# Kernel optimization log

Hardware: AMD Instinct MI355X
Metric: run time of the kernel (lower is better)

The kernel has to match this reference:

```python
import jax, jax.numpy as jnp
import numpy as np


def setup_inputs() -> dict:
    key = jax.random.key(0)
    ks = jax.random.split(key, 8)
    B, S, H, I = 2, 1025, 3200, 12800
    T = B * S
    # int8 tensors represented as int32, symmetric range [-128, 126]
    hidden_states = jax.random.randint(ks[0], (B, S, H), 0, 255, dtype=jnp.int32) - 127
    scale_in = (jax.random.uniform(ks[1], (T,)) * 0.02 + 1e-4).astype(jnp.float16)
    w1 = jax.random.randint(ks[2], (I, H), 0, 255, dtype=jnp.int32) - 127
    w1_scale = (jax.random.uniform(ks[3], (I,)) * 0.01 + 1e-4).astype(jnp.float32)
    b1 = (jax.random.normal(ks[4], (I,)) * 0.02).astype(jnp.float16)
    w2 = jax.random.randint(ks[5], (H, I), 0, 255, dtype=jnp.int32) - 127
    w2_scale = (jax.random.uniform(ks[6], (H,)) * 0.01 + 1e-4).astype(jnp.float32)
    b2 = (jax.random.normal(ks[7], (H,)) * 0.02).astype(jnp.float16)
    return {"hidden_states": hidden_states, "scale_in": scale_in,
            "w1": w1, "w1_scale": w1_scale, "b1": b1,
            "w2": w2, "w2_scale": w2_scale, "b2": b2}


def _w8a8_linear(x_int, scale_x, w_int, w_scale, bias):
    # int8 GEMM with int32 accumulation, dequant with per-token * per-channel scales
    acc = jnp.matmul(x_int, w_int.T)  # [T, out] int32
    out = acc.astype(jnp.float32) * scale_x[:, None].astype(jnp.float32) * w_scale[None, :]
    return (out + bias.astype(jnp.float32)).astype(jnp.float16)


def _gelu_and_quant(x_f16):
    # fused GELU + per-token dynamic symmetric int8 quantization
    g = jax.nn.gelu(x_f16.astype(jnp.float32), approximate=False)  # [T, I]
    amax = jnp.max(jnp.abs(g), axis=-1)                              # [T]
    scale_act = (amax / 127.0).astype(jnp.float16)
    s = jnp.maximum(scale_act.astype(jnp.float32), 1e-8)
    q = jnp.clip(jnp.round(g / s[:, None]), -128, 127).astype(jnp.int32)
    return q, scale_act


def reference(hidden_states, scale_in, w1, w1_scale, b1, w2, w2_scale, b2):
    B, S, H = hidden_states.shape
    x = hidden_states.reshape(-1, H)               # [T, H] int
    fc1_out = _w8a8_linear(x, scale_in, w1, w1_scale, b1)      # [T, I] fp16
    act_out, scale_act = _gelu_and_quant(fc1_out)              # int8-as-int32, [T] fp16
    fc2_out = _w8a8_linear(act_out, scale_act, w2, w2_scale, b2)  # [T, H] fp16
    return fc2_out
```

## Files before the change

### kernel.cpp

```cpp
#include <hip/hip_runtime.h>
#include <hip/hip_fp16.h>

typedef int v4i __attribute__((ext_vector_type(4)));

#define AS1C(p) ((const __attribute__((address_space(1))) void*)(p))
#define AS3(p)  ((__attribute__((address_space(3))) void*)(p))

__device__ __forceinline__ void stage_tile(const signed char* __restrict__ g, long long ld,
                                           long long rmax, long long r0, int k0,
                                           char* lds, int tid) {
  const int wave = tid >> 6, lane = tid & 63;
#pragma unroll
  for (int p = 0; p < 2; ++p) {
    const int chunk = wave * 2 + p;
    const int row = chunk * 16 + (lane >> 2);
    const int slot = lane & 3;
    const int gslot = slot ^ ((row >> 1) & 3);
    long long rg = r0 + row;
    if (rg > rmax) rg = rmax;
    const signed char* src = g + rg * ld + (long long)k0 + gslot * 16;
    char* dst = lds + chunk * 1024;
    __builtin_amdgcn_global_load_lds(AS1C(src), AS3(dst), 16, 0, 0);
  }
}

template <int EPI>
__launch_bounds__(256, 4)
__global__ void gemm_i8(const signed char* __restrict__ A, const signed char* __restrict__ Bw,
                        int M, int N, int K,
                        const float* __restrict__ scale_tok, const float* __restrict__ wsc,
                        const float* __restrict__ bias,
                        __half* __restrict__ gout, unsigned int* __restrict__ amax,
                        float* __restrict__ fout) {
  __shared__ __align__(16) char lds[2][2][128 * 64];
  const int tid = threadIdx.x;
  const int lane = tid & 63, wave = tid >> 6;
  const int wrow = (wave >> 1) * 64, wcol = (wave & 1) * 64;

  const int gy = gridDim.y;
  int lid;
  {
    const int o = blockIdx.y * gridDim.x + blockIdx.x;
    const int nwg = gridDim.x * gy;
    const int q = nwg >> 3, r = nwg & 7;
    const int x = o & 7, p = o >> 3;
    lid = (x < r ? x * (q + 1) : r * (q + 1) + (x - r) * q) + p;
  }
  const long long t0 = (long long)(lid % gy) * 128;
  const long long n0 = (long long)(lid / gy) * 128;

  v4i acc[4][4] = {};

  stage_tile(A, K, (long long)M - 1, t0, 0, lds[0][0], tid);
  stage_tile(Bw, K, (long long)N - 1, n0, 0, lds[0][1], tid);
  __syncthreads();

  const int nk = K >> 6;
  int cur = 0;
  const int srow = lane & 15, sseg = lane >> 4;
  for (int kt = 0; kt < nk; ++kt) {
    if (kt + 1 < nk) {
      stage_tile(A, K, (long long)M - 1, t0, (kt + 1) << 6, lds[cur ^ 1][0], tid);
      stage_tile(Bw, K, (long long)N - 1, n0, (kt + 1) << 6, lds[cur ^ 1][1], tid);
    }
    v4i af[4], bf[4];
#pragma unroll
    for (int mi = 0; mi < 4; ++mi) {
      const int r = wrow + mi * 16 + srow;
      const int sl = sseg ^ ((r >> 1) & 3);
      af[mi] = *(const v4i*)&lds[cur][0][r * 64 + sl * 16];
    }
#pragma unroll
    for (int ni = 0; ni < 4; ++ni) {
      const int r = wcol + ni * 16 + srow;
      const int sl = sseg ^ ((r >> 1) & 3);
      bf[ni] = *(const v4i*)&lds[cur][1][r * 64 + sl * 16];
    }
#pragma unroll
    for (int mi = 0; mi < 4; ++mi)
#pragma unroll
      for (int ni = 0; ni < 4; ++ni)
        acc[mi][ni] = __builtin_amdgcn_mfma_i32_16x16x64_i8(af[mi], bf[ni], acc[mi][ni], 0, 0, 0);
    __syncthreads();
    cur ^= 1;
  }

  if (EPI == 0) {
#pragma unroll
    for (int mi = 0; mi < 4; ++mi) {
#pragma unroll
      for (int j = 0; j < 4; ++j) {
        const long long t = t0 + wrow + mi * 16 + (lane >> 4) * 4 + j;
        const bool valid = (t < M);
        const float st = valid ? scale_tok[t] : 0.f;
        float rowmax = 0.f;
#pragma unroll
        for (int ni = 0; ni < 4; ++ni) {
          const long long c = n0 + wcol + ni * 16 + (lane & 15);
          float v = (float)acc[mi][ni][j] * st * wsc[c] + bias[c];
          v = __half2float(__float2half(v));
          const float gl = 0.5f * v * (1.f + erff(v * 0.70710678118654752f));
          rowmax = fmaxf(rowmax, fabsf(gl));
          if (valid) gout[t * (long long)N + c] = __float2half(gl);
        }
#pragma unroll
        for (int m = 1; m < 16; m <<= 1) rowmax = fmaxf(rowmax, __shfl_xor(rowmax, m));
        if (valid && (lane & 15) == 0) atomicMax(&amax[t], __float_as_uint(rowmax));
      }
    }
  } else {
#pragma unroll
    for (int mi = 0; mi < 4; ++mi) {
#pragma unroll
      for (int j = 0; j < 4; ++j) {
        const long long t = t0 + wrow + mi * 16 + (lane >> 4) * 4 + j;
        if (t < M) {
          const float am = __uint_as_float(amax[t]);
          const float st = __half2float(__float2half(am * (1.f / 127.f)));
#pragma unroll
          for (int ni = 0; ni < 4; ++ni) {
            const long long c = n0 + wcol + ni * 16 + (lane & 15);
            const float v = (float)acc[mi][ni][j] * st * wsc[c] + bias[c];
            fout[t * (long long)N + c] = __half2float(__float2half(v));
          }
        }
      }
    }
  }
}

__global__ void pack_all(const int* __restrict__ a, const int* __restrict__ b,
                         const int* __restrict__ c,
                         signed char* __restrict__ pa, signed char* __restrict__ pb,
                         signed char* __restrict__ pc,
                         unsigned int* __restrict__ amax,
                         long long na, long long nb, long long nc, int T) {
  const long long gid = blockIdx.x * (long long)blockDim.x + threadIdx.x;
  if (gid < T) amax[gid] = 0u;
  const long long n4a = na >> 2, n4b = nb >> 2, n4c = nc >> 2;
  const long long tot = n4a + n4b + n4c;
  const long long stride = (long long)gridDim.x * blockDim.x;
  for (long long u = gid; u < tot; u += stride) {
    const int* src; signed char* dst; long long loc;
    if (u < n4a)            { src = a; dst = pa; loc = u; }
    else if (u < n4a + n4b) { src = b; dst = pb; loc = u - n4a; }
    else                    { src = c; dst = pc; loc = u - n4a - n4b; }
    const int4 v = *(const int4*)(src + (loc << 2));
    const unsigned out = (unsigned)(v.x & 0xff) | ((unsigned)(v.y & 0xff) << 8) |
                         ((unsigned)(v.z & 0xff) << 16) | ((unsigned)(v.w & 0xff) << 24);
    *(unsigned*)(dst + (loc << 2)) = out;
  }
}

__global__ void gelu_quant(const __half* __restrict__ g, const unsigned int* __restrict__ amax,
                           signed char* __restrict__ q, long long total, int I) {
  const long long nchunk = total >> 3;
  const long long stride = (long long)gridDim.x * blockDim.x;
  for (long long c = blockIdx.x * (long long)blockDim.x + threadIdx.x; c < nchunk; c += stride) {
    const long long base = c << 3;
    const int t = (int)(base / I);
    const float am = __uint_as_float(amax[t]);
    const float s = fmaxf(__half2float(__float2half(am * (1.f / 127.f))), 1e-8f);
    const float inv = 1.f / s;
    const int4 raw = *(const int4*)(g + base);
    const __half2* h2 = (const __half2*)&raw;
    union { signed char b[8]; int2 v; } u;
#pragma unroll
    for (int k = 0; k < 4; ++k) {
      const float2 f = __half22float2(h2[k]);
      const float q0 = fminf(fmaxf(rintf(f.x * inv), -128.f), 127.f);
      const float q1 = fminf(fmaxf(rintf(f.y * inv), -128.f), 127.f);
      u.b[k * 2]     = (signed char)(int)q0;
      u.b[k * 2 + 1] = (signed char)(int)q1;
    }
    *(int2*)(q + base) = u.v;
  }
}

extern "C" void kernel_launch(void* const* d_in, const int* in_sizes, int n_in,
                              void* d_out, int out_size, void* d_ws, size_t ws_size,
                              hipStream_t stream) {
  const int* hs = (const int*)d_in[0];
  const float* scale_in = (const float*)d_in[1];
  const int* w1 = (const int*)d_in[2];
  const float* w1s = (const float*)d_in[3];
  const float* b1 = (const float*)d_in[4];
  const int* w2 = (const int*)d_in[5];
  const float* w2s = (const float*)d_in[6];
  const float* b2 = (const float*)d_in[7];

  const int T = in_sizes[1];
  const int I = in_sizes[3];
  const int H = in_sizes[6];

  char* ws = (char*)d_ws;
  unsigned int* amax = (unsigned int*)ws;
  signed char* px  = (signed char*)(ws + 16384);
  signed char* pw1 = px + (size_t)T * H;
  signed char* pw2 = pw1 + (size_t)I * H;
  __half* gbuf = (__half*)(pw2 + (size_t)H * I);
  signed char* qbuf = (signed char*)(gbuf + (size_t)T * I);

  const long long nx = (long long)T * H, nw1 = (long long)I * H, nw2 = (long long)H * I;

  pack_all<<<2048, 256, 0, stream>>>(hs, w1, w2, px, pw1, pw2, amax, nx, nw1, nw2, T);

  dim3 g1(I / 128, (T + 127) / 128);
  gemm_i8<0><<<g1, 256, 0, stream>>>(px, pw1, T, I, H, scale_in, w1s, b1, gbuf, amax, nullptr);

  gelu_quant<<<2048, 256, 0, stream>>>(gbuf, amax, qbuf, (long long)T * I, I);

  dim3 g2(H / 128, (T + 127) / 128);
  gemm_i8<1><<<g2, 256, 0, stream>>>(qbuf, pw2, T, H, I, nullptr, w2s, b2, nullptr, amax, (float*)d_out);
}
```

Baseline: 380.0 us.

## Reshape GEMM tiles to 64x256 with waves splitting columns and precomputed load pointers

Changes each GEMM workgroup tile from 128x128 to 64 tokens by 256 output channels. All four waves now share the same A rows and each owns a 64-column slice of B. Global-to-LDS staging uses precomputed, incrementally advanced pointers instead of recomputing addresses each k-step, and per-column scale and bias are hoisted out of the epilogue. The tile is aimed at this skinny-M shape: it lowers tile padding waste for T=2050 and changes the A/B traffic ratio. In exchange, B must be re-read from global memory more often (more row tiles), N-bound checks are added for H not divisible by 256, and LDS use per block rises.

Result: slower. 423.9 us (+11.5%).

```diff
diff --git a/kernel.cpp b/kernel.cpp
--- a/kernel.cpp
+++ b/kernel.cpp
@@ -6,36 +6,18 @@
 #define AS1C(p) ((const __attribute__((address_space(1))) void*)(p))
 #define AS3(p)  ((__attribute__((address_space(3))) void*)(p))
 
-__device__ __forceinline__ void stage_tile(const signed char* __restrict__ g, long long ld,
-                                           long long rmax, long long r0, int k0,
-                                           char* lds, int tid) {
-  const int wave = tid >> 6, lane = tid & 63;
-#pragma unroll
-  for (int p = 0; p < 2; ++p) {
-    const int chunk = wave * 2 + p;
-    const int row = chunk * 16 + (lane >> 2);
-    const int slot = lane & 3;
-    const int gslot = slot ^ ((row >> 1) & 3);
-    long long rg = r0 + row;
-    if (rg > rmax) rg = rmax;
-    const signed char* src = g + rg * ld + (long long)k0 + gslot * 16;
-    char* dst = lds + chunk * 1024;
-    __builtin_amdgcn_global_load_lds(AS1C(src), AS3(dst), 16, 0, 0);
-  }
-}
-
 template <int EPI>
 __launch_bounds__(256, 4)
-__global__ void gemm_i8(const signed char* __restrict__ A, const signed char* __restrict__ Bw,
-                        int M, int N, int K,
-                        const float* __restrict__ scale_tok, const float* __restrict__ wsc,
-                        const float* __restrict__ bias,
-                        __half* __restrict__ gout, unsigned int* __restrict__ amax,
-                        float* __restrict__ fout) {
-  __shared__ __align__(16) char lds[2][2][128 * 64];
+__global__ void gemm_w(const signed char* __restrict__ A, const signed char* __restrict__ Bw,
+                       int M, int N, int K,
+                       const float* __restrict__ scale_tok, const float* __restrict__ wsc,
+                       const float* __restrict__ bias,
+                       __half* __restrict__ gout, unsigned int* __restrict__ amax,
+                       float* __restrict__ fout) {
+  __shared__ __align__(16) char smem[2][20480];
   const int tid = threadIdx.x;
   const int lane = tid & 63, wave = tid >> 6;
-  const int wrow = (wave >> 1) * 64, wcol = (wave & 1) * 64;
+  const int lh = lane & 15, sseg = lane >> 4;
 
   const int gy = gridDim.y;
   int lid;
@@ -46,36 +28,56 @@
     const int x = o & 7, p = o >> 3;
     lid = (x < r ? x * (q + 1) : r * (q + 1) + (x - r) * q) + p;
   }
-  const long long t0 = (long long)(lid % gy) * 128;
-  const long long n0 = (long long)(lid / gy) * 128;
+  const long long t0 = (long long)(lid % gy) * 64;
+  const long long n0 = (long long)(lid / gy) * 256;
+  const int nk = K >> 6;
+  const long long Mm1 = M - 1, Nm1 = N - 1;
+
+  const int lr4 = lane >> 2, slot = lane & 3;
+  const signed char* spA;
+  {
+    const int rloc = wave * 16 + lr4;
+    const int gslot = (slot ^ ((rloc >> 1) & 3)) << 4;
+    long long gr = t0 + rloc; if (gr > Mm1) gr = Mm1;
+    spA = A + gr * (long long)K + gslot;
+  }
+  const signed char* spB[4];
+#pragma unroll
+  for (int i = 0; i < 4; ++i) {
+    const int cb = wave * 4 + i;
+    const int rloc = cb * 16 + lr4;
+    const int gslot = (slot ^ ((rloc >> 1) & 3)) << 4;
+    long long gr = n0 + rloc; if (gr > Nm1) gr = Nm1;
+    spB[i] = Bw + gr * (long long)K + gslot;
+  }
+  const int dstA = wave * 1024;
+
+#define STAGE(bi) do { \
+    __builtin_amdgcn_global_load_lds(AS1C(spA), AS3(&smem[bi][dstA]), 16, 0, 0); spA += 64; \
+    _Pragma("unroll") \
+    for (int i = 0; i < 4; ++i) { \
+      __builtin_amdgcn_global_load_lds(AS1C(spB[i]), AS3(&smem[bi][4096 + (wave * 4 + i) * 1024]), 16, 0, 0); \
+      spB[i] += 64; \
+    } \
+  } while (0)
+
+  const int xs = ((sseg ^ ((lh >> 1) & 3)) << 4);
+  const int offA = lh * 64 + xs;
+  const int offB = 4096 + wave * 4096 + lh * 64 + xs;
 
   v4i acc[4][4] = {};
 
-  stage_tile(A, K, (long long)M - 1, t0, 0, lds[0][0], tid);
-  stage_tile(Bw, K, (long long)N - 1, n0, 0, lds[0][1], tid);
+  STAGE(0);
   __syncthreads();
 
-  const int nk = K >> 6;
   int cur = 0;
-  const int srow = lane & 15, sseg = lane >> 4;
   for (int kt = 0; kt < nk; ++kt) {
-    if (kt + 1 < nk) {
-      stage_tile(A, K, (long long)M - 1, t0, (kt + 1) << 6, lds[cur ^ 1][0], tid);
-      stage_tile(Bw, K, (long long)N - 1, n0, (kt + 1) << 6, lds[cur ^ 1][1], tid);
-    }
+    if (kt + 1 < nk) STAGE(cur ^ 1);
     v4i af[4], bf[4];
 #pragma unroll
-    for (int mi = 0; mi < 4; ++mi) {
-      const int r = wrow + mi * 16 + srow;
-      const int sl = sseg ^ ((r >> 1) & 3);
-      af[mi] = *(const v4i*)&lds[cur][0][r * 64 + sl * 16];
-    }
-#pragma unroll
-    for (int ni = 0; ni < 4; ++ni) {
-      const int r = wcol + ni * 16 + srow;
-      const int sl = sseg ^ ((r >> 1) & 3);
-      bf[ni] = *(const v4i*)&lds[cur][1][r * 64 + sl * 16];
-    }
+    for (int mi = 0; mi < 4; ++mi) af[mi] = *(const v4i*)&smem[cur][offA + mi * 1024];
+#pragma unroll
+    for (int ni = 0; ni < 4; ++ni) bf[ni] = *(const v4i*)&smem[cur][offB + ni * 1024];
 #pragma unroll
     for (int mi = 0; mi < 4; ++mi)
 #pragma unroll
@@ -84,28 +86,36 @@
     __syncthreads();
     cur ^= 1;
   }
-
+#undef STAGE
+
+  long long cidx[4]; float w4[4], bi4[4]; bool cok[4];
+#pragma unroll
+  for (int ni = 0; ni < 4; ++ni) {
+    cidx[ni] = n0 + wave * 64 + ni * 16 + lh;
+    cok[ni] = cidx[ni] < N;
+    w4[ni] = cok[ni] ? wsc[cidx[ni]] : 0.f;
+    bi4[ni] = cok[ni] ? bias[cidx[ni]] : 0.f;
+  }
   if (EPI == 0) {
 #pragma unroll
     for (int mi = 0; mi < 4; ++mi) {
 #pragma unroll
       for (int j = 0; j < 4; ++j) {
-        const long long t = t0 + wrow + mi * 16 + (lane >> 4) * 4 + j;
+        const long long t = t0 + mi * 16 + (lane >> 4) * 4 + j;
         const bool valid = (t < M);
         const float st = valid ? scale_tok[t] : 0.f;
         float rowmax = 0.f;
 #pragma unroll
         for (int ni = 0; ni < 4; ++ni) {
-          const long long c = n0 + wcol + ni * 16 + (lane & 15);
-          float v = (float)acc[mi][ni][j] * st * wsc[c] + bias[c];
+          float v = (float)acc[mi][ni][j] * st * w4[ni] + bi4[ni];
           v = __half2float(__float2half(v));
           const float gl = 0.5f * v * (1.f + erff(v * 0.70710678118654752f));
           rowmax = fmaxf(rowmax, fabsf(gl));
-          if (valid) gout[t * (long long)N + c] = __float2half(gl);
+          if (valid && cok[ni]) gout[t * (long long)N + cidx[ni]] = __float2half(gl);
         }
 #pragma unroll
         for (int m = 1; m < 16; m <<= 1) rowmax = fmaxf(rowmax, __shfl_xor(rowmax, m));
-        if (valid && (lane & 15) == 0) atomicMax(&amax[t], __float_as_uint(rowmax));
+        if (valid && lh == 0) atomicMax(&amax[t], __float_as_uint(rowmax));
       }
     }
   } else {
@@ -113,15 +123,14 @@
     for (int mi = 0; mi < 4; ++mi) {
 #pragma unroll
       for (int j = 0; j < 4; ++j) {
-        const long long t = t0 + wrow + mi * 16 + (lane >> 4) * 4 + j;
+        const long long t = t0 + mi * 16 + (lane >> 4) * 4 + j;
         if (t < M) {
           const float am = __uint_as_float(amax[t]);
           const float st = __half2float(__float2half(am * (1.f / 127.f)));
 #pragma unroll
           for (int ni = 0; ni < 4; ++ni) {
-            const long long c = n0 + wcol + ni * 16 + (lane & 15);
-            const float v = (float)acc[mi][ni][j] * st * wsc[c] + bias[c];
-            fout[t * (long long)N + c] = __half2float(__float2half(v));
+            const float v = (float)acc[mi][ni][j] * st * w4[ni] + bi4[ni];
+            if (cok[ni]) fout[t * (long long)N + cidx[ni]] = __half2float(__float2half(v));
           }
         }
       }
@@ -205,11 +214,11 @@
 
   pack_all<<<2048, 256, 0, stream>>>(hs, w1, w2, px, pw1, pw2, amax, nx, nw1, nw2, T);
 
-  dim3 g1(I / 128, (T + 127) / 128);
-  gemm_i8<0><<<g1, 256, 0, stream>>>(px, pw1, T, I, H, scale_in, w1s, b1, gbuf, amax, nullptr);
+  dim3 g1(I / 256, (T + 63) / 64);
+  gemm_w<0><<<g1, 256, 0, stream>>>(px, pw1, T, I, H, scale_in, w1s, b1, gbuf, amax, nullptr);
 
   gelu_quant<<<2048, 256, 0, stream>>>(gbuf, amax, qbuf, (long long)T * I, I);
 
-  dim3 g2(H / 128, (T + 127) / 128);
-  gemm_i8<1><<<g2, 256, 0, stream>>>(qbuf, pw2, T, H, I, nullptr, w2s, b2, nullptr, amax, (float*)d_out);
-}
+  dim3 g2((H + 255) / 256, (T + 63) / 64);
+  gemm_w<1><<<g2, 256, 0, stream>>>(qbuf, pw2, T, H, I, nullptr, w2s, b2, nullptr, amax, (float*)d_out);
+}
```

## Use 256x256 tiles with 1024-thread blocks for the FC1 GEMM

Applied to the files above, without the earlier changes.

Replaces the FC1 int8 GEMM with a new kernel that computes 256x256 output tiles using 16 waves, each wave still holding a 64x64 accumulator block. Larger tiles halve the global traffic per MAC and make each LDS stage reuse more data. Staging pointers are precomputed and advanced by a stride. Per-column scale and bias are hoisted out of the epilogue loop. The risks are fewer workgroups (about 9x50) for the 256 CUs, a tail in the last M tile where T=2050 is padded to 2304, and higher LDS use per block (64 KB). FC2 keeps the old kernel, now specialised without the template.

After: 374.7 us. About the same (-1.4%).

```diff
diff --git a/kernel.cpp b/kernel.cpp
--- a/kernel.cpp
+++ b/kernel.cpp
@@ -5,6 +5,116 @@
 
 #define AS1C(p) ((const __attribute__((address_space(1))) void*)(p))
 #define AS3(p)  ((__attribute__((address_space(3))) void*)(p))
+
+__launch_bounds__(1024, 4)
+__global__ void gemm256(const signed char* __restrict__ A, const signed char* __restrict__ Bw,
+                        int M, int N, int K,
+                        const float* __restrict__ scale_tok, const float* __restrict__ wsc,
+                        const float* __restrict__ bias,
+                        __half* __restrict__ gout, unsigned int* __restrict__ amax) {
+  __shared__ __align__(16) char smem[2][32768];
+  const int tid = threadIdx.x;
+  const int lane = tid & 63, wave = tid >> 6;
+  const int wavem = wave >> 2, waven = wave & 3;
+  const int lh = lane & 15, sseg = lane >> 4;
+
+  const int gy = gridDim.y;
+  int lid;
+  {
+    const int o = blockIdx.y * gridDim.x + blockIdx.x;
+    const int nwg = gridDim.x * gy;
+    const int q = nwg >> 3, r = nwg & 7;
+    const int x = o & 7, p = o >> 3;
+    lid = (x < r ? x * (q + 1) : r * (q + 1) + (x - r) * q) + p;
+  }
+  const long long t0 = (long long)(lid % gy) * 256;
+  const long long n0 = (long long)(lid / gy) * 256;
+  const int nk = K >> 6;
+  const long long Mm1 = M - 1, Nm1 = N - 1;
+
+  const int lr4 = lane >> 2, slot = lane & 3;
+  const int rloc = wave * 16 + lr4;
+  const int gslot = (slot ^ ((rloc >> 1) & 3)) << 4;
+  const signed char* sp0;
+  const signed char* sp1;
+  {
+    long long gr = t0 + rloc; if (gr > Mm1) gr = Mm1;
+    sp0 = A + gr * (long long)K + gslot;
+    long long gn = n0 + rloc; if (gn > Nm1) gn = Nm1;
+    sp1 = Bw + gn * (long long)K + gslot;
+  }
+  const int d0 = wave * 1024, d1 = 16384 + wave * 1024;
+
+#define STAGE(bi) do { \
+    __builtin_amdgcn_global_load_lds(AS1C(sp0), AS3(&smem[bi][d0]), 16, 0, 0); sp0 += 64; \
+    __builtin_amdgcn_global_load_lds(AS1C(sp1), AS3(&smem[bi][d1]), 16, 0, 0); sp1 += 64; \
+  } while (0)
+
+  const int xs = ((sseg ^ ((lh >> 1) & 3)) << 4);
+  const int offA = wavem * 4096 + lh * 64 + xs;
+  const int offB = 16384 + waven * 4096 + lh * 64 + xs;
+
+  v4i acc[4][4] = {};
+
+  STAGE(0);
+  __syncthreads();
+
+  int cur = 0;
+  for (int kt = 0; kt < nk; ++kt) {
+    if (kt + 1 < nk) STAGE(cur ^ 1);
+    const char* base = smem[cur];
+    v4i af[4], bf[2];
+#pragma unroll
+    for (int mi = 0; mi < 4; ++mi) af[mi] = *(const v4i*)(base + offA + mi * 1024);
+    bf[0] = *(const v4i*)(base + offB);
+    bf[1] = *(const v4i*)(base + offB + 1024);
+#pragma unroll
+    for (int mi = 0; mi < 4; ++mi) {
+      acc[mi][0] = __builtin_amdgcn_mfma_i32_16x16x64_i8(af[mi], bf[0], acc[mi][0], 0, 0, 0);
+      acc[mi][1] = __builtin_amdgcn_mfma_i32_16x16x64_i8(af[mi], bf[1], acc[mi][1], 0, 0, 0);
+    }
+    bf[0] = *(const v4i*)(base + offB + 2048);
+    bf[1] = *(const v4i*)(base + offB + 3072);
+#pragma unroll
+    for (int mi = 0; mi < 4; ++mi) {
+      acc[mi][2] = __builtin_amdgcn_mfma_i32_16x16x64_i8(af[mi], bf[0], acc[mi][2], 0, 0, 0);
+      acc[mi][3] = __builtin_amdgcn_mfma_i32_16x16x64_i8(af[mi], bf[1], acc[mi][3], 0, 0, 0);
+    }
+    __syncthreads();
+    cur ^= 1;
+  }
+#undef STAGE
+
+  long long cidx[4]; float w4[4], bi4[4]; bool cok[4];
+#pragma unroll
+  for (int ni = 0; ni < 4; ++ni) {
+    cidx[ni] = n0 + waven * 64 + ni * 16 + lh;
+    cok[ni] = cidx[ni] < N;
+    w4[ni] = cok[ni] ? wsc[cidx[ni]] : 0.f;
+    bi4[ni] = cok[ni] ? bias[cidx[ni]] : 0.f;
+  }
+#pragma unroll
+  for (int mi = 0; mi < 4; ++mi) {
+#pragma unroll
+    for (int j = 0; j < 4; ++j) {
+      const long long t = t0 + wavem * 64 + mi * 16 + (lane >> 4) * 4 + j;
+      const bool valid = t < M;
+      const float st = valid ? scale_tok[t] : 0.f;
+      float rowmax = 0.f;
+#pragma unroll
+      for (int ni = 0; ni < 4; ++ni) {
+        float v = (float)acc[mi][ni][j] * st * w4[ni] + bi4[ni];
+        v = __half2float(__float2half(v));
+        const float gl = 0.5f * v * (1.f + erff(v * 0.70710678118654752f));
+        rowmax = fmaxf(rowmax, fabsf(gl));
+        if (valid && cok[ni]) gout[t * (long long)N + cidx[ni]] = __float2half(gl);
+      }
+#pragma unroll
+      for (int m = 1; m < 16; m <<= 1) rowmax = fmaxf(rowmax, __shfl_xor(rowmax, m));
+      if (valid && lh == 0) atomicMax(&amax[t], __float_as_uint(rowmax));
+    }
+  }
+}
 
 __device__ __forceinline__ void stage_tile(const signed char* __restrict__ g, long long ld,
                                            long long rmax, long long r0, int k0,
@@ -24,14 +134,11 @@
   }
 }
 
-template <int EPI>
 __launch_bounds__(256, 4)
-__global__ void gemm_i8(const signed char* __restrict__ A, const signed char* __restrict__ Bw,
-                        int M, int N, int K,
-                        const float* __restrict__ scale_tok, const float* __restrict__ wsc,
-                        const float* __restrict__ bias,
-                        __half* __restrict__ gout, unsigned int* __restrict__ amax,
-                        float* __restrict__ fout) {
+__global__ void gemm_fc2(const signed char* __restrict__ A, const signed char* __restrict__ Bw,
+                         int M, int N, int K,
+                         const float* __restrict__ wsc, const float* __restrict__ bias,
+                         unsigned int* __restrict__ amax, float* __restrict__ fout) {
   __shared__ __align__(16) char lds[2][2][128 * 64];
   const int tid = threadIdx.x;
   const int lane = tid & 63, wave = tid >> 6;
@@ -85,44 +192,19 @@
     cur ^= 1;
   }
 
-  if (EPI == 0) {
-#pragma unroll
-    for (int mi = 0; mi < 4; ++mi) {
-#pragma unroll
-      for (int j = 0; j < 4; ++j) {
-        const long long t = t0 + wrow + mi * 16 + (lane >> 4) * 4 + j;
-        const bool valid = (t < M);
-        const float st = valid ? scale_tok[t] : 0.f;
-        float rowmax = 0.f;
+#pragma unroll
+  for (int mi = 0; mi < 4; ++mi) {
+#pragma unroll
+    for (int j = 0; j < 4; ++j) {
+      const long long t = t0 + wrow + mi * 16 + (lane >> 4) * 4 + j;
+      if (t < M) {
+        const float am = __uint_as_float(amax[t]);
+        const float st = __half2float(__float2half(am * (1.f / 127.f)));
 #pragma unroll
         for (int ni = 0; ni < 4; ++ni) {
           const long long c = n0 + wcol + ni * 16 + (lane & 15);
-          float v = (float)acc[mi][ni][j] * st * wsc[c] + bias[c];
-          v = __half2float(__float2half(v));
-          const float gl = 0.5f * v * (1.f + erff(v * 0.70710678118654752f));
-          rowmax = fmaxf(rowmax, fabsf(gl));
-          if (valid) gout[t * (long long)N + c] = __float2half(gl);
-        }
-#pragma unroll
-        for (int m = 1; m < 16; m <<= 1) rowmax = fmaxf(rowmax, __shfl_xor(rowmax, m));
-        if (valid && (lane & 15) == 0) atomicMax(&amax[t], __float_as_uint(rowmax));
-      }
-    }
-  } else {
-#pragma unroll
-    for (int mi = 0; mi < 4; ++mi) {
-#pragma unroll
-      for (int j = 0; j < 4; ++j) {
-        const long long t = t0 + wrow + mi * 16 + (lane >> 4) * 4 + j;
-        if (t < M) {
-          const float am = __uint_as_float(amax[t]);
-          const float st = __half2float(__float2half(am * (1.f / 127.f)));
-#pragma unroll
-          for (int ni = 0; ni < 4; ++ni) {
-            const long long c = n0 + wcol + ni * 16 + (lane & 15);
-            const float v = (float)acc[mi][ni][j] * st * wsc[c] + bias[c];
-            fout[t * (long long)N + c] = __half2float(__float2half(v));
-          }
+          const float v = (float)acc[mi][ni][j] * st * wsc[c] + bias[c];
+          fout[t * (long long)N + c] = __half2float(__float2half(v));
         }
       }
     }
@@ -205,11 +287,11 @@
 
   pack_all<<<2048, 256, 0, stream>>>(hs, w1, w2, px, pw1, pw2, amax, nx, nw1, nw2, T);
 
-  dim3 g1(I / 128, (T + 127) / 128);
-  gemm_i8<0><<<g1, 256, 0, stream>>>(px, pw1, T, I, H, scale_in, w1s, b1, gbuf, amax, nullptr);
+  dim3 g1(I / 256, (T + 255) / 256);
+  gemm256<<<g1, 1024, 0, stream>>>(px, pw1, T, I, H, scale_in, w1s, b1, gbuf, amax);
 
   gelu_quant<<<2048, 256, 0, stream>>>(gbuf, amax, qbuf, (long long)T * I, I);
 
   dim3 g2(H / 128, (T + 127) / 128);
-  gemm_i8<1><<<g2, 256, 0, stream>>>(qbuf, pw2, T, H, I, nullptr, w2s, b2, nullptr, amax, (float*)d_out);
-}
+  gemm_fc2<<<g2, 256, 0, stream>>>(qbuf, pw2, T, H, I, w2s, b2, amax, (float*)d_out);
+}
```
